# Kernel tuning notes

Hardware: AMD Instinct MI355X
Metric: run time of the kernel (lower is better)

The kernel has to match this reference:

```python
import jax, jax.numpy as jnp
import numpy as np

EPS = 1e-12  # matches F.normalize clamp


def sparsemax(z):
    # Martins & Astudillo sparsemax along the last axis
    K = z.shape[-1]
    z_sorted = -jnp.sort(-z, axis=-1)                      # descending
    k = jnp.arange(1, K + 1, dtype=z.dtype)
    z_cum = jnp.cumsum(z_sorted, axis=-1)
    support = (1.0 + k * z_sorted) > z_cum                 # [..., K]
    k_z = jnp.sum(support, axis=-1, keepdims=True)         # support size
    tau = (jnp.take_along_axis(z_cum, k_z - 1, axis=-1) - 1.0) / k_z.astype(z.dtype)
    return jnp.maximum(z - tau, 0.0)


def setup_inputs() -> dict:
    key = jax.random.key(0)
    k1, k2, k3 = jax.random.split(key, 3)
    B, IN, OUT = 8192, 512, 4096
    x = jax.random.normal(k1, (B, IN), dtype=jnp.float32)
    weight = jax.random.normal(k2, (OUT, IN), dtype=jnp.float32)
    lambd = jnp.square(jax.random.normal(k3, (1,), dtype=jnp.float32))  # torch init: randn**2
    return {"x": x, "weight": weight, "lambd": lambd}


def reference(x, weight, lambd):
    # normalize prototypes and inputs onto the unit hypersphere
    w_n = weight / jnp.maximum(jnp.linalg.norm(weight, axis=-1, keepdims=True), EPS)
    x_n = x / jnp.maximum(jnp.linalg.norm(x, axis=1, keepdims=True), EPS)
    xa = x_n @ w_n.T                                        # [B, OUT]
    # ||x - a||^2 via Gram expansion (avoids [B, OUT, IN] broadcast tensor)
    x2 = jnp.sum(x_n * x_n, axis=-1, keepdims=True)         # [B, 1]
    w2 = jnp.sum(w_n * w_n, axis=-1)                        # [OUT]
    sq_dist = x2 + w2[None, :] - 2.0 * xa                   # [B, OUT]
    logits = xa - lambd * sq_dist                           # kds_mode='recon_dist'
    return sparsemax(logits)
```

## Files before the change

kernel.cpp:

```cpp
#include <hip/hip_runtime.h>

typedef __attribute__((ext_vector_type(8))) short bf16x8;
typedef __attribute__((ext_vector_type(4))) float f32x4;

__device__ inline unsigned short f2bf(float f) {
  union { float f; unsigned u; } v; v.f = f;
  unsigned r = v.u + 0x7FFFu + ((v.u >> 16) & 1u);
  return (unsigned short)(r >> 16);
}

__global__ __launch_bounds__(256) void normalize_both(
    const float* __restrict__ x, const float* __restrict__ wgt,
    unsigned short* __restrict__ xb, unsigned short* __restrict__ wb) {
  const int w = threadIdx.x >> 6, lane = threadIdx.x & 63;
  const int row = blockIdx.x * 4 + w;
  const float* src;
  unsigned short* dst;
  if (row < 8192) { src = x + (size_t)row * 512;           dst = xb + (size_t)row * 512; }
  else            { src = wgt + (size_t)(row - 8192) * 512; dst = wb + (size_t)(row - 8192) * 512; }
  const float* p = src + lane * 8;
  float4 a = *reinterpret_cast<const float4*>(p);
  float4 b = *reinterpret_cast<const float4*>(p + 4);
  float ss = a.x*a.x + a.y*a.y + a.z*a.z + a.w*a.w
           + b.x*b.x + b.y*b.y + b.z*b.z + b.w*b.w;
  #pragma unroll
  for (int off = 32; off; off >>= 1) ss += __shfl_xor(ss, off);
  const float inv = 1.0f / fmaxf(sqrtf(ss), 1e-12f);
  unsigned short o[8];
  o[0]=f2bf(a.x*inv); o[1]=f2bf(a.y*inv); o[2]=f2bf(a.z*inv); o[3]=f2bf(a.w*inv);
  o[4]=f2bf(b.x*inv); o[5]=f2bf(b.y*inv); o[6]=f2bf(b.z*inv); o[7]=f2bf(b.w*inv);
  *reinterpret_cast<uint4*>(dst + lane * 8) = *reinterpret_cast<uint4*>(o);
}

#define BM 256
#define BN 256
#define BK 32

#define STAGE_A(slot_, ko_, j_)                                                   \
  do {                                                                            \
    const int c_ = wid * 2 + (j_);                                                \
    const unsigned short* s_ = Xb + (size_t)(bm0 + c_ * 16 + srow) * 512 + (ko_) + sskel; \
    __builtin_amdgcn_global_load_lds(                                             \
        (const __attribute__((address_space(1))) void*)s_,                        \
        (__attribute__((address_space(3))) void*)&As[slot_][c_ * 512], 16, 0, 0); \
  } while (0)
#define STAGE_B(slot_, ko_, j_)                                                   \
  do {                                                                            \
    const int c_ = wid * 2 + (j_);                                                \
    const unsigned short* s_ = Wb + (size_t)(bn0 + c_ * 16 + srow) * 512 + (ko_) + sskel; \
    __builtin_amdgcn_global_load_lds(                                             \
        (const __attribute__((address_space(1))) void*)s_,                        \
        (__attribute__((address_space(3))) void*)&Bs[slot_][c_ * 512], 16, 0, 0); \
  } while (0)

__global__ __launch_bounds__(512, 2) void gemm_logits_f16(
    const unsigned short* __restrict__ Xb, const unsigned short* __restrict__ Wb,
    const float* __restrict__ lambd, unsigned short* __restrict__ out16) {
  __shared__ unsigned short As[3][BM * BK];
  __shared__ unsigned short Bs[3][BN * BK];
  const int tid = threadIdx.x, lane = tid & 63, wid = tid >> 6;
  const int wm = wid >> 2, wn = wid & 3;
  const int lrow = lane & 15, kg = lane >> 4;

  const int id = (int)blockIdx.x;
  const int swz = (id & 7) * 64 + (id >> 3);
  const int bx = swz & 15;
  const int by = swz >> 4;
  const int bm0 = by * BM, bn0 = bx * BN;

  const int srow  = lane >> 2;
  const int sskel = ((lane & 3) ^ ((lane >> 3) & 3)) * 8;

  const int rswz = (lrow >> 1) & 3;
  const int kA = (kg ^ rswz) * 8;

  f32x4 acc[8][4];
  #pragma unroll
  for (int m = 0; m < 8; ++m)
    #pragma unroll
    for (int n = 0; n < 4; ++n) { f32x4 z = {0.f,0.f,0.f,0.f}; acc[m][n] = z; }

  STAGE_A(0, 0, 0); STAGE_A(0, 0, 1); STAGE_B(0, 0, 0); STAGE_B(0, 0, 1);
  STAGE_A(1, BK, 0); STAGE_A(1, BK, 1); STAGE_B(1, BK, 0); STAGE_B(1, BK, 1);
  asm volatile("s_waitcnt vmcnt(4)" ::: "memory");
  __builtin_amdgcn_s_barrier();
  __builtin_amdgcn_sched_barrier(0);

  #pragma unroll
  for (int t = 0; t < 16; ++t) {
    const int cur = t % 3, nx2 = (t + 2) % 3;
    if (t + 2 < 16) { STAGE_A(nx2, (t + 2) * BK, 0); STAGE_A(nx2, (t + 2) * BK, 1); }
    bf16x8 af0[4], bfr[4];
    #pragma unroll
    for (int mf = 0; mf < 4; ++mf)
      af0[mf] = *reinterpret_cast<const bf16x8*>(
          &As[cur][(wm * 128 + mf * 16 + lrow) * BK + kA]);
    #pragma unroll
    for (int nf = 0; nf < 4; ++nf)
      bfr[nf] = *reinterpret_cast<const bf16x8*>(
          &Bs[cur][(wn * 64 + nf * 16 + lrow) * BK + kA]);
    asm volatile("s_waitcnt lgkmcnt(0)" ::: "memory");
    __builtin_amdgcn_sched_barrier(0);
    __builtin_amdgcn_s_setprio(1);
    #pragma unroll
    for (int mf = 0; mf < 4; ++mf)
      #pragma unroll
      for (int nf = 0; nf < 4; ++nf)
        acc[mf][nf] = __builtin_amdgcn_mfma_f32_16x16x32_bf16(
            af0[mf], bfr[nf], acc[mf][nf], 0, 0, 0);
    __builtin_amdgcn_s_setprio(0);
    __builtin_amdgcn_sched_barrier(0);
    if (t + 2 < 16) { STAGE_B(nx2, (t + 2) * BK, 0); STAGE_B(nx2, (t + 2) * BK, 1); }
    bf16x8 af1[4];
    #pragma unroll
    for (int mf = 0; mf < 4; ++mf)
      af1[mf] = *reinterpret_cast<const bf16x8*>(
          &As[cur][(wm * 128 + 64 + mf * 16 + lrow) * BK + kA]);
    asm volatile("s_waitcnt lgkmcnt(0)" ::: "memory");
    __builtin_amdgcn_sched_barrier(0);
    __builtin_amdgcn_s_setprio(1);
    #pragma unroll
    for (int mf = 0; mf < 4; ++mf)
      #pragma unroll
      for (int nf = 0; nf < 4; ++nf)
        acc[mf + 4][nf] = __builtin_amdgcn_mfma_f32_16x16x32_bf16(
            af1[mf], bfr[nf], acc[mf + 4][nf], 0, 0, 0);
    __builtin_amdgcn_s_setprio(0);
    __builtin_amdgcn_sched_barrier(0);
    if (t < 15) {
      if (t < 13) { asm volatile("s_waitcnt vmcnt(4)" ::: "memory"); }
      else        { asm volatile("s_waitcnt vmcnt(0)" ::: "memory"); }
      __builtin_amdgcn_s_barrier();
      __builtin_amdgcn_sched_barrier(0);
    }
  }

  const float lam = lambd[0];
  const float sa_ = 1.0f + 2.0f * lam, sb_ = 2.0f * lam;
  #pragma unroll
  for (int mf = 0; mf < 8; ++mf) {
    #pragma unroll
    for (int nf = 0; nf < 4; ++nf) {
      const int gc = bn0 + wn * 64 + nf * 16 + lrow;
      #pragma unroll
      for (int r = 0; r < 4; ++r) {
        const int gr = bm0 + wm * 128 + mf * 16 + kg * 4 + r;
        union { _Float16 h; unsigned short u; } cv;
        cv.h = (_Float16)(sa_ * acc[mf][nf][r] - sb_);
        out16[(size_t)gr * 4096 + gc] = cv.u;
      }
    }
  }
}

__global__ __launch_bounds__(256) void sparsemax_f16(
    const unsigned short* __restrict__ zin, float* __restrict__ out) {
  const int tid = threadIdx.x;
  const unsigned short* zr = zin + (size_t)blockIdx.x * 4096;
  float* orow = out + (size_t)blockIdx.x * 4096;

  float v[16];
  #pragma unroll
  for (int b = 0; b < 2; ++b) {
    uint4 pk = *reinterpret_cast<const uint4*>(&zr[b * 2048 + tid * 8]);
    const unsigned short* ph = reinterpret_cast<const unsigned short*>(&pk);
    #pragma unroll
    for (int j = 0; j < 8; ++j) {
      union { unsigned short u; _Float16 h; } cv; cv.u = ph[j];
      v[b * 8 + j] = (float)cv.h;
    }
  }

  __shared__ float sred[2][4];
  __shared__ int   cred[2][4];
  const int lane = tid & 63, w = tid >> 6;

  float ls = 0.f;
  #pragma unroll
  for (int j = 0; j < 16; ++j) ls += v[j];
  #pragma unroll
  for (int off = 32; off; off >>= 1) ls += __shfl_xor(ls, off);
  if (lane == 0) sred[0][w] = ls;
  __syncthreads();
  float tau = (sred[0][0] + sred[0][1] + sred[0][2] + sred[0][3] - 1.0f)
              * (1.0f / 4096.0f);
  int prevC = 4096;

  for (int it = 0; it < 32; ++it) {
    const int pw = 1 - (it & 1);
    float s = 0.f; int c = 0;
    #pragma unroll
    for (int j = 0; j < 16; ++j) { if (v[j] > tau) { s += v[j]; ++c; } }
    #pragma unroll
    for (int off = 32; off; off >>= 1) { s += __shfl_xor(s, off); c += __shfl_xor(c, off); }
    if (lane == 0) { sred[pw][w] = s; cred[pw][w] = c; }
    __syncthreads();
    const float S = sred[pw][0] + sred[pw][1] + sred[pw][2] + sred[pw][3];
    const int   C = cred[pw][0] + cred[pw][1] + cred[pw][2] + cred[pw][3];
    tau = (S - 1.0f) / (float)C;
    if (C == prevC) break;
    prevC = C;
  }

  #pragma unroll
  for (int b = 0; b < 2; ++b) {
    float4 t0, t1;
    t0.x = fmaxf(v[b*8+0] - tau, 0.f);
    t0.y = fmaxf(v[b*8+1] - tau, 0.f);
    t0.z = fmaxf(v[b*8+2] - tau, 0.f);
    t0.w = fmaxf(v[b*8+3] - tau, 0.f);
    t1.x = fmaxf(v[b*8+4] - tau, 0.f);
    t1.y = fmaxf(v[b*8+5] - tau, 0.f);
    t1.z = fmaxf(v[b*8+6] - tau, 0.f);
    t1.w = fmaxf(v[b*8+7] - tau, 0.f);
    *reinterpret_cast<float4*>(&orow[b * 2048 + tid * 8])     = t0;
    *reinterpret_cast<float4*>(&orow[b * 2048 + tid * 8 + 4]) = t1;
  }
}

extern "C" void kernel_launch(void* const* d_in, const int* in_sizes, int n_in,
                              void* d_out, int out_size, void* d_ws, size_t ws_size,
                              hipStream_t stream) {
  const float* x     = (const float*)d_in[0];
  const float* wgt   = (const float*)d_in[1];
  const float* lambd = (const float*)d_in[2];
  float* out = (float*)d_out;

  unsigned short* xb  = (unsigned short*)d_ws;
  unsigned short* wb  = xb + (size_t)8192 * 512;
  unsigned short* z16 = wb + (size_t)4096 * 512;

  normalize_both<<<(8192 + 4096) / 4, 256, 0, stream>>>(x, wgt, xb, wb);

  gemm_logits_f16<<<512, 512, 0, stream>>>(xb, wb, lambd, z16);

  sparsemax_f16<<<8192, 256, 0, stream>>>(z16, out);
}
```

Measured before the change: 111.7 us.

## Process each sparsemax row with a single wavefront instead of a block

Reassigns sparsemax work so that one 64-lane wave owns a full 4096-element row (64 values per lane), with four rows per block. The shared-memory cross-wave reduction and the __syncthreads in every fixed-point iteration go away, leaving only wave shuffles. In exchange each lane holds 64 floats in registers and loops over four times as many elements per iteration, which can lower occupancy and lengthen the serial per-iteration work.

```diff
diff --git a/kernel.cpp b/kernel.cpp
--- a/kernel.cpp
+++ b/kernel.cpp
@@ -153,68 +153,57 @@
   }
 }
 
-__global__ __launch_bounds__(256) void sparsemax_f16(
+__global__ __launch_bounds__(256) void sparsemax_wave(
     const unsigned short* __restrict__ zin, float* __restrict__ out) {
-  const int tid = threadIdx.x;
-  const unsigned short* zr = zin + (size_t)blockIdx.x * 4096;
-  float* orow = out + (size_t)blockIdx.x * 4096;
-
-  float v[16];
-  #pragma unroll
-  for (int b = 0; b < 2; ++b) {
-    uint4 pk = *reinterpret_cast<const uint4*>(&zr[b * 2048 + tid * 8]);
+  const int lane = threadIdx.x & 63;
+  const int row  = ((int)blockIdx.x << 2) + (threadIdx.x >> 6);
+  const unsigned short* zr = zin + (size_t)row * 4096;
+  float* orow = out + (size_t)row * 4096;
+
+  float v[64];
+  #pragma unroll
+  for (int c = 0; c < 8; ++c) {
+    uint4 pk = *reinterpret_cast<const uint4*>(&zr[c * 512 + lane * 8]);
     const unsigned short* ph = reinterpret_cast<const unsigned short*>(&pk);
     #pragma unroll
     for (int j = 0; j < 8; ++j) {
       union { unsigned short u; _Float16 h; } cv; cv.u = ph[j];
-      v[b * 8 + j] = (float)cv.h;
+      v[c * 8 + j] = (float)cv.h;
     }
   }
 
-  __shared__ float sred[2][4];
-  __shared__ int   cred[2][4];
-  const int lane = tid & 63, w = tid >> 6;
-
   float ls = 0.f;
   #pragma unroll
-  for (int j = 0; j < 16; ++j) ls += v[j];
+  for (int j = 0; j < 64; ++j) ls += v[j];
   #pragma unroll
   for (int off = 32; off; off >>= 1) ls += __shfl_xor(ls, off);
-  if (lane == 0) sred[0][w] = ls;
-  __syncthreads();
-  float tau = (sred[0][0] + sred[0][1] + sred[0][2] + sred[0][3] - 1.0f)
-              * (1.0f / 4096.0f);
+  float tau = (ls - 1.0f) * (1.0f / 4096.0f);
   int prevC = 4096;
 
   for (int it = 0; it < 32; ++it) {
-    const int pw = 1 - (it & 1);
     float s = 0.f; int c = 0;
     #pragma unroll
-    for (int j = 0; j < 16; ++j) { if (v[j] > tau) { s += v[j]; ++c; } }
+    for (int j = 0; j < 64; ++j) { if (v[j] > tau) { s += v[j]; ++c; } }
     #pragma unroll
     for (int off = 32; off; off >>= 1) { s += __shfl_xor(s, off); c += __shfl_xor(c, off); }
-    if (lane == 0) { sred[pw][w] = s; cred[pw][w] = c; }
-    __syncthreads();
-    const float S = sred[pw][0] + sred[pw][1] + sred[pw][2] + sred[pw][3];
-    const int   C = cred[pw][0] + cred[pw][1] + cred[pw][2] + cred[pw][3];
-    tau = (S - 1.0f) / (float)C;
-    if (C == prevC) break;
-    prevC = C;
-  }
-
-  #pragma unroll
-  for (int b = 0; b < 2; ++b) {
+    tau = (s - 1.0f) / (float)c;
+    if (c == prevC) break;
+    prevC = c;
+  }
+
+  #pragma unroll
+  for (int c = 0; c < 8; ++c) {
     float4 t0, t1;
-    t0.x = fmaxf(v[b*8+0] - tau, 0.f);
-    t0.y = fmaxf(v[b*8+1] - tau, 0.f);
-    t0.z = fmaxf(v[b*8+2] - tau, 0.f);
-    t0.w = fmaxf(v[b*8+3] - tau, 0.f);
-    t1.x = fmaxf(v[b*8+4] - tau, 0.f);
-    t1.y = fmaxf(v[b*8+5] - tau, 0.f);
-    t1.z = fmaxf(v[b*8+6] - tau, 0.f);
-    t1.w = fmaxf(v[b*8+7] - tau, 0.f);
-    *reinterpret_cast<float4*>(&orow[b * 2048 + tid * 8])     = t0;
-    *reinterpret_cast<float4*>(&orow[b * 2048 + tid * 8 + 4]) = t1;
+    t0.x = fmaxf(v[c*8+0] - tau, 0.f);
+    t0.y = fmaxf(v[c*8+1] - tau, 0.f);
+    t0.z = fmaxf(v[c*8+2] - tau, 0.f);
+    t0.w = fmaxf(v[c*8+3] - tau, 0.f);
+    t1.x = fmaxf(v[c*8+4] - tau, 0.f);
+    t1.y = fmaxf(v[c*8+5] - tau, 0.f);
+    t1.z = fmaxf(v[c*8+6] - tau, 0.f);
+    t1.w = fmaxf(v[c*8+7] - tau, 0.f);
+    *reinterpret_cast<float4*>(&orow[c * 512 + lane * 8])     = t0;
+    *reinterpret_cast<float4*>(&orow[c * 512 + lane * 8 + 4]) = t1;
   }
 }
 
@@ -234,5 +223,5 @@
 
   gemm_logits_f16<<<512, 512, 0, stream>>>(xb, wb, lambd, z16);
 
-  sparsemax_f16<<<8192, 256, 0, stream>>>(z16, out);
-}
+  sparsemax_wave<<<8192 / 4, 256, 0, stream>>>(z16, out);
+}
```

After: 95.26 us, median of 2. 1.17x faster.
